# Kernel tuning notes

Hardware: AMD Instinct MI355X
Metric: run time of the kernel (lower is better)

The kernel has to match this reference:

```python
import jax, jax.numpy as jnp
import numpy as np

B, S, H = 128, 512, 768      # batch, seq, encoder hidden
NL = 42                      # len(LABEL_TO_ID)
LD = 300                     # label_dim
DK, DV = 64, 768             # K_dim, V_dim
HID = 768                    # opt['hidden_dim']
P = 512                      # max_seq_length == pos_indicator
INF = 1e12                   # constant.INFINITY_NUMBER
NEG = -1e9


def gelu(x):
    return 0.5 * x * (1.0 + jax.lax.erf(x * 0.7071067811865476))


def setup_inputs() -> dict:
    key = jax.random.key(0)
    ks = jax.random.split(key, 24)
    sc = 0.02
    return {
        "inputs": jax.random.normal(ks[0], (B, S, H), jnp.float32),
        "pos_ids": jax.random.randint(ks[1], (B, S), 0, 53),
        "dep_ids": jax.random.randint(ks[2], (B, S), 0, 42),
        "subj_pos": jax.random.randint(ks[3], (B, S), 0, P + 1),
        "obj_pos": jax.random.randint(ks[4], (B, S), 0, P + 1),
        "adj": jnp.zeros((1, 1, 1), jnp.float32),  # unused by forward
        # stacked per-label Q/K projections (41 = NL-1 labels, label 0 excluded)
        "WQ": jax.random.normal(ks[5], (NL - 1, DK, H), jnp.float32) * sc,
        "bQ": jax.random.normal(ks[6], (NL - 1, DK), jnp.float32) * sc,
        "WK": jax.random.normal(ks[7], (NL - 1, DK, LD), jnp.float32) * sc,
        "bK": jax.random.normal(ks[8], (NL - 1, DK), jnp.float32) * sc,
        "WV_w": jax.random.normal(ks[9], (DV, H), jnp.float32) * sc,
        "WV_b": jax.random.normal(ks[10], (DV,), jnp.float32) * sc,
        "Wout_w": jax.random.normal(ks[11], (H, DV), jnp.float32) * sc,
        "Wout_b": jax.random.normal(ks[12], (H,), jnp.float32) * sc,
        "ln_g": jnp.ones((H,), jnp.float32),
        "ln_b": jnp.zeros((H,), jnp.float32),
        "label_emb": jax.random.normal(ks[13], (NL, LD), jnp.float32) * sc,
        "feat_w": jax.random.normal(ks[14], (HID, 3 * H), jnp.float32) * sc,
        "feat_b": jax.random.normal(ks[15], (HID,), jnp.float32) * sc,
        "out_w": jax.random.normal(ks[16], (LD, HID), jnp.float32) * sc,
        "out_b": jax.random.normal(ks[17], (LD,), jnp.float32) * sc,
    }


def reference(inputs, pos_ids, dep_ids, subj_pos, obj_pos, adj,
              WQ, bQ, WK, bK, WV_w, WV_b, Wout_w, Wout_b, ln_g, ln_b,
              label_emb, feat_w, feat_b, out_w, out_b):
    dt = inputs.dtype
    # combined attention mask (bool OR, as torch bool+bool): entity markers + padding
    mask = (subj_pos == P) | (obj_pos == P) | (pos_ids == 0)   # [B,S]

    # --- LabelAttention: 41-loop collapses to one fused projection ---
    lab = label_emb[1:NL]                                      # [41,LD] labels 1..41
    kvec = jnp.einsum('ld,lkd->lk', lab, WK) + bK              # [41,DK] per-label keys
    # scores_sum[b,s] = sum_l (x W_Q_l^T + b_Q_l) . k_l  /sqrt(dk)  + 41*mask*NEG
    w_eff = jnp.einsum('lk,lkh->h', kvec, WQ)                  # [H]
    c = jnp.sum(kvec * bQ)                                     # scalar
    scores = (inputs @ w_eff + c) / 8.0                        # sqrt(DK)=8; [B,S]
    scores = scores + (NL - 1) * mask.astype(dt) * NEG
    attn = jax.nn.softmax(scores, axis=-1)                     # [B,S]

    wv = inputs @ WV_w.T + WV_b                                # [B,S,DV]
    ctx = jnp.einsum('bs,bsd->bd', attn, wv)                   # [B,DV]
    ctx = gelu(ctx @ Wout_w.T + Wout_b)                        # [B,H]
    mu = ctx.mean(-1, keepdims=True)
    var = ((ctx - mu) ** 2).mean(-1, keepdims=True)
    ctx = (ctx - mu) / jnp.sqrt(var + 1e-5) * ln_g + ln_b

    # --- entity max pooling (mask True where NOT part of entity) ---
    sm = (subj_pos != P)[:, :, None]
    om = (obj_pos != P)[:, :, None]
    subj_out = jnp.where(sm, -INF, inputs).max(axis=1)         # [B,H]
    obj_out = jnp.where(om, -INF, inputs).max(axis=1)          # [B,H]

    feats = jnp.concatenate([subj_out, obj_out, ctx], axis=-1)  # [B,3H]
    feats = gelu(feats @ feat_w.T + feat_b)                     # [B,HID]
    feats = gelu(feats @ out_w.T + out_b)                       # [B,LD]

    logits = feats @ label_emb.T                                # [B,42]
    return logits, ctx
```

## Files before the change

### kernel.cpp

```cpp
#include <hip/hip_runtime.h>
#include <math.h>

#define BB 128
#define SS 512
#define HH 768
#define PPOS 512
#define NEGC (-1.0e9f)
#define NINF (-1.0e12f)

#define OFF_KVEC   0
#define OFF_WEFF   2624
#define OFF_C      3392
#define OFF_CAT    0
#define OFF_POOLED 294912
#define OFF_PP     393216
#define OFF_PS     1179648
#define OFF_PO     1966080
#define OFF_PZ     2752512
#define OFF_CTXA   393216
#define OFF_CTXB   491520
#define OFF_F1     589824
#define OFF_F2     688128

__device__ __forceinline__ float gelu_f(float x) {
    return 0.5f * x * (1.0f + erff(x * 0.70710678118654752f));
}
__device__ __forceinline__ float dot4(float4 a, float4 b) {
    return a.x*b.x + a.y*b.y + a.z*b.z + a.w*b.w;
}

template<int K4, int ACT, int MT>
__global__ __launch_bounds__(256) void k_mm(const float* __restrict__ A,
        const float* __restrict__ W, const float* __restrict__ bias,
        float* __restrict__ C, int M, int N) {
    int lane = threadIdx.x & 63;
    int wave = (blockIdx.x * 256 + threadIdx.x) >> 6;
    int ntn = (N + 15) >> 4;
    int m0 = (wave / ntn) * MT;
    if (m0 >= M) return;
    int n0 = ((wave % ntn) << 4) + (lane >> 2);
    int ks = lane & 3;
    bool nvalid = (n0 < N);
    const float4* A4 = (const float4*)A;
    const float4* w_row = (const float4*)W + (size_t)(nvalid ? n0 : 0) * K4;
    const float4* ar = A4 + (size_t)m0 * K4;
    float acc[MT];
    #pragma unroll
    for (int r = 0; r < MT; ++r) acc[r] = 0.f;
    #pragma unroll 4
    for (int j = ks; j < K4; j += 4) {
        float4 wv = w_row[j];
        #pragma unroll
        for (int r = 0; r < MT; ++r) acc[r] += dot4(ar[(size_t)r * K4 + j], wv);
    }
    #pragma unroll
    for (int r = 0; r < MT; ++r) {
        acc[r] += __shfl_xor(acc[r], 1, 64);
        acc[r] += __shfl_xor(acc[r], 2, 64);
    }
    if (ks == 0 && nvalid) {
        float b = bias ? bias[n0] : 0.f;
        #pragma unroll
        for (int r = 0; r < MT; ++r) {
            float v = acc[r] + b;
            if (ACT == 1) v = gelu_f(v);
            C[(size_t)(m0 + r) * N + n0] = v;
        }
    }
}

template<int K4, int ACT>
__global__ __launch_bounds__(256) void k_mmX(const float* __restrict__ A,
        const float* __restrict__ W, const float* __restrict__ bias,
        float* __restrict__ C) {
    int lane = threadIdx.x & 63, wave = threadIdx.x >> 6;
    int x = blockIdx.x & 7;
    int k = blockIdx.x >> 3;
    int nb = x * 6 + (k % 6);
    int mb = k / 6;
    int m0 = mb * 8 + wave * 2;
    int n_sub = lane >> 2, ks = lane & 3;
    int n0 = (nb << 4) + n_sub;
    const float4* w_row = (const float4*)W + (size_t)n0 * K4;
    const float4* ar = (const float4*)A + (size_t)m0 * K4;
    float acc0 = 0.f, acc1 = 0.f;
    #pragma unroll 4
    for (int j = ks; j < K4; j += 4) {
        float4 wv = w_row[j];
        acc0 += dot4(ar[j], wv);
        acc1 += dot4(ar[K4 + j], wv);
    }
    acc0 += __shfl_xor(acc0, 1, 64); acc0 += __shfl_xor(acc0, 2, 64);
    acc1 += __shfl_xor(acc1, 1, 64); acc1 += __shfl_xor(acc1, 2, 64);
    if (ks == 0) {
        float b = bias ? bias[n0] : 0.f;
        float v0 = acc0 + b, v1 = acc1 + b;
        if (ACT == 1) { v0 = gelu_f(v0); v1 = gelu_f(v1); }
        C[(size_t)m0 * HH + n0] = v0;
        C[(size_t)(m0 + 1) * HH + n0] = v1;
    }
}

__global__ __launch_bounds__(256) void k_kvec2(const float* __restrict__ label_emb,
        const float* __restrict__ WK, const float* __restrict__ bK,
        float* __restrict__ ws) {
    if (blockIdx.x < 3) ws[OFF_WEFF + blockIdx.x * 256 + threadIdx.x] = 0.f;
    if (blockIdx.x == 3 && threadIdx.x == 0) ws[OFF_C] = 0.f;
    int lane = threadIdx.x & 63;
    int idx = (blockIdx.x * 256 + threadIdx.x) >> 6;
    int l = idx >> 6;
    const float4* lab4 = (const float4*)(label_emb + (size_t)(l + 1) * 300);
    const float4* wk4  = (const float4*)(WK + (size_t)idx * 300);
    float acc = dot4(lab4[lane], wk4[lane]);
    if (lane < 11) acc += dot4(lab4[64 + lane], wk4[64 + lane]);
    #pragma unroll
    for (int off = 32; off > 0; off >>= 1) acc += __shfl_xor(acc, off, 64);
    if (lane == 0) ws[OFF_KVEC + idx] = acc + bK[idx];
}

__global__ __launch_bounds__(256) void k_weff2(const float* __restrict__ WQ,
        const float* __restrict__ bQ, float* __restrict__ ws) {
    int lane = threadIdx.x & 63;
    int w = (blockIdx.x * 256 + threadIdx.x) >> 6;
    if (w < 492) {
        int jc = w / 12, hg = w % 12;
        int h = hg * 64 + lane;
        const float* wq = WQ + (size_t)(jc * 64) * HH + h;
        const float* kv = ws + OFF_KVEC + jc * 64;
        float acc = 0.f;
        #pragma unroll 8
        for (int j = 0; j < 64; ++j) acc += kv[j] * wq[(size_t)j * HH];
        atomicAdd(&ws[OFF_WEFF + h], acc);
    } else if (w == 492) {
        float acc = 0.f;
        for (int j = lane; j < 2624; j += 64) acc += ws[OFF_KVEC + j] * bQ[j];
        #pragma unroll
        for (int off = 32; off > 0; off >>= 1) acc += __shfl_xor(acc, off, 64);
        if (lane == 0) atomicAdd(&ws[OFF_C], acc);
    }
}

__global__ __launch_bounds__(256) void k_fused(const float* __restrict__ inputs,
        const int* __restrict__ pos_ids, const int* __restrict__ subj_pos,
        const int* __restrict__ obj_pos, float* __restrict__ ws) {
    __shared__ float l_pe[4][768];
    __shared__ float l_sm[4][768];
    __shared__ float l_om[4][768];
    __shared__ float l_z[4];
    __shared__ int l_mask[64];
    int chunk = blockIdx.x, b = blockIdx.y;
    int t = threadIdx.x, wave = t >> 6, lane = t & 63;
    int row0 = b * SS + chunk * 64;
    if (t < 64) {
        int g = row0 + t;
        int sp = subj_pos[g], op = obj_pos[g], pi = pos_ids[g];
        int m = ((sp == PPOS) | (op == PPOS) | (pi == 0)) ? 1 : 0;
        if (sp == PPOS) m |= 2;
        if (op == PPOS) m |= 4;
        l_mask[t] = m;
    }
    const float4* w4 = (const float4*)(ws + OFF_WEFF);
    float c = ws[OFF_C];
    float4 w0 = w4[lane], w1 = w4[64 + lane], w2 = w4[128 + lane];
    __syncthreads();
    const float4* in4 = (const float4*)inputs;
    float4 pe0 = make_float4(0.f, 0.f, 0.f, 0.f);
    float4 pe1 = pe0, pe2 = pe0;
    float4 sm0 = make_float4(NINF, NINF, NINF, NINF);
    float4 sm1 = sm0, sm2 = sm0, om0 = sm0, om1 = sm0, om2 = sm0;
    float z = 0.f;
    int rbase = wave * 16;
    #pragma unroll 4
    for (int r = 0; r < 16; ++r) {
        int s = rbase + r;
        const float4* x4 = in4 + (size_t)(row0 + s) * 192;
        float4 x0 = x4[lane], x1 = x4[64 + lane], x2 = x4[128 + lane];
        float acc = dot4(x0, w0) + dot4(x1, w1) + dot4(x2, w2);
        #pragma unroll
        for (int off = 32; off > 0; off >>= 1) acc += __shfl_xor(acc, off, 64);
        int mk = l_mask[s];
        float e = (mk & 1) ? 0.f : __expf((acc + c) * 0.125f);
        z += e;
        pe0.x += e * x0.x; pe0.y += e * x0.y; pe0.z += e * x0.z; pe0.w += e * x0.w;
        pe1.x += e * x1.x; pe1.y += e * x1.y; pe1.z += e * x1.z; pe1.w += e * x1.w;
        pe2.x += e * x2.x; pe2.y += e * x2.y; pe2.z += e * x2.z; pe2.w += e * x2.w;
        if (mk & 2) {
            sm0.x = fmaxf(sm0.x, x0.x); sm0.y = fmaxf(sm0.y, x0.y);
            sm0.z = fmaxf(sm0.z, x0.z); sm0.w = fmaxf(sm0.w, x0.w);
            sm1.x = fmaxf(sm1.x, x1.x); sm1.y = fmaxf(sm1.y, x1.y);
            sm1.z = fmaxf(sm1.z, x1.z); sm1.w = fmaxf(sm1.w, x1.w);
            sm2.x = fmaxf(sm2.x, x2.x); sm2.y = fmaxf(sm2.y, x2.y);
            sm2.z = fmaxf(sm2.z, x2.z); sm2.w = fmaxf(sm2.w, x2.w);
        }
        if (mk & 4) {
            om0.x = fmaxf(om0.x, x0.x); om0.y = fmaxf(om0.y, x0.y);
            om0.z = fmaxf(om0.z, x0.z); om0.w = fmaxf(om0.w, x0.w);
            om1.x = fmaxf(om1.x, x1.x); om1.y = fmaxf(om1.y, x1.y);
            om1.z = fmaxf(om1.z, x1.z); om1.w = fmaxf(om1.w, x1.w);
            om2.x = fmaxf(om2.x, x2.x); om2.y = fmaxf(om2.y, x2.y);
            om2.z = fmaxf(om2.z, x2.z); om2.w = fmaxf(om2.w, x2.w);
        }
    }
    ((float4*)l_pe[wave])[lane] = pe0;
    ((float4*)l_pe[wave])[64 + lane] = pe1;
    ((float4*)l_pe[wave])[128 + lane] = pe2;
    ((float4*)l_sm[wave])[lane] = sm0;
    ((float4*)l_sm[wave])[64 + lane] = sm1;
    ((float4*)l_sm[wave])[128 + lane] = sm2;
    ((float4*)l_om[wave])[lane] = om0;
    ((float4*)l_om[wave])[64 + lane] = om1;
    ((float4*)l_om[wave])[128 + lane] = om2;
    if (lane == 0) l_z[wave] = z;
    __syncthreads();
    if (t < 192) {
        float4 p = make_float4(0.f, 0.f, 0.f, 0.f);
        float4 s = make_float4(NINF, NINF, NINF, NINF);
        float4 o = s;
        #pragma unroll
        for (int w = 0; w < 4; ++w) {
            float4 vp = ((float4*)l_pe[w])[t];
            float4 vs = ((float4*)l_sm[w])[t];
            float4 vo = ((float4*)l_om[w])[t];
            p.x += vp.x; p.y += vp.y; p.z += vp.z; p.w += vp.w;
            s.x = fmaxf(s.x, vs.x); s.y = fmaxf(s.y, vs.y);
            s.z = fmaxf(s.z, vs.z); s.w = fmaxf(s.w, vs.w);
            o.x = fmaxf(o.x, vo.x); o.y = fmaxf(o.y, vo.y);
            o.z = fmaxf(o.z, vo.z); o.w = fmaxf(o.w, vo.w);
        }
        size_t oo = (size_t)(b * 8 + chunk) * 192 + t;
        ((float4*)(ws + OFF_PP))[oo] = p;
        ((float4*)(ws + OFF_PS))[oo] = s;
        ((float4*)(ws + OFF_PO))[oo] = o;
    }
    if (t == 0) ws[OFF_PZ + b * 8 + chunk] = l_z[0] + l_z[1] + l_z[2] + l_z[3];
}

__global__ void k_reduce(float* __restrict__ ws) {
    int i = blockIdx.x * 256 + threadIdx.x;
    int b = i / HH, h = i - b * HH;
    float p = 0.f, sm = NINF, om = NINF, zt = 0.f;
    #pragma unroll
    for (int j = 0; j < 8; ++j) {
        int o = (b * 8 + j) * HH + h;
        p += ws[OFF_PP + o];
        sm = fmaxf(sm, ws[OFF_PS + o]);
        om = fmaxf(om, ws[OFF_PO + o]);
        zt += ws[OFF_PZ + b * 8 + j];
    }
    ws[OFF_POOLED + i] = p / zt;
    ws[OFF_CAT + (size_t)b * 2304 + h] = sm;
    ws[OFF_CAT + (size_t)b * 2304 + 768 + h] = om;
}

__global__ void k_ln(const float* __restrict__ ln_g, const float* __restrict__ ln_b,
                     float* __restrict__ ws, float* __restrict__ out) {
    __shared__ float red[256];
    __shared__ float red2[256];
    int b = blockIdx.x, t = threadIdx.x;
    const float* x = ws + OFF_CTXB + (size_t)b * HH;
    float a0 = x[t], a1 = x[t + 256], a2 = x[t + 512];
    red[t]  = a0 + a1 + a2;
    red2[t] = a0 * a0 + a1 * a1 + a2 * a2;
    __syncthreads();
    for (int s2 = 128; s2 > 0; s2 >>= 1) {
        if (t < s2) { red[t] += red[t + s2]; red2[t] += red2[t + s2]; }
        __syncthreads();
    }
    float mu  = red[0] * (1.0f / 768.0f);
    float var = red2[0] * (1.0f / 768.0f) - mu * mu;
    float inv = rsqrtf(var + 1e-5f);
    float* o = out + 5376 + (size_t)b * HH;
    float* cc = ws + OFF_CAT + (size_t)b * 2304 + 1536;
    float r0 = (a0 - mu) * inv * ln_g[t]       + ln_b[t];
    float r1 = (a1 - mu) * inv * ln_g[t + 256] + ln_b[t + 256];
    float r2 = (a2 - mu) * inv * ln_g[t + 512] + ln_b[t + 512];
    o[t] = r0; o[t + 256] = r1; o[t + 512] = r2;
    cc[t] = r0; cc[t + 256] = r1; cc[t + 512] = r2;
}

extern "C" void kernel_launch(void* const* d_in, const int* in_sizes, int n_in,
                              void* d_out, int out_size, void* d_ws, size_t ws_size,
                              hipStream_t stream) {
    const float* inputs    = (const float*)d_in[0];
    const int*   pos_ids   = (const int*)d_in[1];
    const int*   subj_pos  = (const int*)d_in[3];
    const int*   obj_pos   = (const int*)d_in[4];
    const float* WQ        = (const float*)d_in[6];
    const float* bQ        = (const float*)d_in[7];
    const float* WK        = (const float*)d_in[8];
    const float* bK        = (const float*)d_in[9];
    const float* WV_w      = (const float*)d_in[10];
    const float* WV_b      = (const float*)d_in[11];
    const float* Wout_w    = (const float*)d_in[12];
    const float* Wout_b    = (const float*)d_in[13];
    const float* ln_g      = (const float*)d_in[14];
    const float* ln_b      = (const float*)d_in[15];
    const float* label_emb = (const float*)d_in[16];
    const float* feat_w    = (const float*)d_in[17];
    const float* feat_b    = (const float*)d_in[18];
    const float* out_w     = (const float*)d_in[19];
    const float* out_b     = (const float*)d_in[20];
    float* out = (float*)d_out;
    float* ws  = (float*)d_ws;

    k_kvec2  <<<656, 256, 0, stream>>>(label_emb, WK, bK, ws);
    k_weff2  <<<124, 256, 0, stream>>>(WQ, bQ, ws);
    k_fused  <<<dim3(8, BB), 256, 0, stream>>>(inputs, pos_ids, subj_pos, obj_pos, ws);
    k_reduce <<<384, 256, 0, stream>>>(ws);
    k_mmX<192,0><<<768, 256, 0, stream>>>(ws + OFF_POOLED, WV_w, WV_b, ws + OFF_CTXA);
    k_mmX<192,1><<<768, 256, 0, stream>>>(ws + OFF_CTXA, Wout_w, Wout_b, ws + OFF_CTXB);
    k_ln     <<<BB, 256, 0, stream>>>(ln_g, ln_b, ws, out);
    k_mmX<576,1><<<768, 256, 0, stream>>>(ws + OFF_CAT, feat_w, feat_b, ws + OFF_F1);
    k_mm<192,1,2><<<304, 256, 0, stream>>>(ws + OFF_F1, out_w, out_b, ws + OFF_F2, BB, 300);
    k_mm<75,0,2><<<48, 256, 0, stream>>>(ws + OFF_F2, label_emb, nullptr, out, BB, 42);
}
```

Measured before the change: 450.2 us.

## Replace partial-buffer reduce kernel with atomic accumulation in fused pass

Removes the k_reduce kernel and its partial buffers. The fused kernel now atomically adds pooled sums and softmax denominators and does an atomicMax on order-preserving uint keys for the entity max pools. Entity max updates are skipped when a chunk has no masked rows. Workspace initialisation moves into the kvec kernel, key decoding into the LN kernel, and division by Z into the first matmul epilogue. This saves one launch and the partial-buffer traffic, at the cost of atomic contention and nondeterministic summation order.

```diff
diff --git a/kernel.cpp b/kernel.cpp
--- a/kernel.cpp
+++ b/kernel.cpp
@@ -5,28 +5,34 @@
 #define SS 512
 #define HH 768
 #define PPOS 512
-#define NEGC (-1.0e9f)
 #define NINF (-1.0e12f)
 
 #define OFF_KVEC   0
 #define OFF_WEFF   2624
 #define OFF_C      3392
-#define OFF_CAT    0
+#define OFF_Z      3456
 #define OFF_POOLED 294912
-#define OFF_PP     393216
-#define OFF_PS     1179648
-#define OFF_PO     1966080
-#define OFF_PZ     2752512
-#define OFF_CTXA   393216
-#define OFF_CTXB   491520
-#define OFF_F1     589824
-#define OFF_F2     688128
+#define OFF_CAT    393216
+#define OFF_CTXA   688128
+#define OFF_CTXB   786432
+#define OFF_F1     884736
+#define OFF_F2     983040
+
+#define N_INIT 295040
+#define INIT_THREADS 167936
 
 __device__ __forceinline__ float gelu_f(float x) {
     return 0.5f * x * (1.0f + erff(x * 0.70710678118654752f));
 }
 __device__ __forceinline__ float dot4(float4 a, float4 b) {
     return a.x*b.x + a.y*b.y + a.z*b.z + a.w*b.w;
+}
+__device__ __forceinline__ unsigned fkey(float f) {
+    unsigned u = __float_as_uint(f);
+    return (u & 0x80000000u) ? ~u : (u | 0x80000000u);
+}
+__device__ __forceinline__ float fkey_dec(unsigned k) {
+    return __uint_as_float((k & 0x80000000u) ? (k & 0x7fffffffu) : ~k);
 }
 
 template<int K4, int ACT, int MT>
@@ -72,7 +78,7 @@
 template<int K4, int ACT>
 __global__ __launch_bounds__(256) void k_mmX(const float* __restrict__ A,
         const float* __restrict__ W, const float* __restrict__ bias,
-        float* __restrict__ C) {
+        float* __restrict__ C, const float* __restrict__ Zv) {
     int lane = threadIdx.x & 63, wave = threadIdx.x >> 6;
     int x = blockIdx.x & 7;
     int k = blockIdx.x >> 3;
@@ -94,7 +100,14 @@
     acc1 += __shfl_xor(acc1, 1, 64); acc1 += __shfl_xor(acc1, 2, 64);
     if (ks == 0) {
         float b = bias ? bias[n0] : 0.f;
-        float v0 = acc0 + b, v1 = acc1 + b;
+        float v0, v1;
+        if (Zv) {
+            v0 = acc0 * (1.f / Zv[m0]) + b;
+            v1 = acc1 * (1.f / Zv[m0 + 1]) + b;
+        } else {
+            v0 = acc0 + b;
+            v1 = acc1 + b;
+        }
         if (ACT == 1) { v0 = gelu_f(v0); v1 = gelu_f(v1); }
         C[(size_t)m0 * HH + n0] = v0;
         C[(size_t)(m0 + 1) * HH + n0] = v1;
@@ -106,6 +119,17 @@
         float* __restrict__ ws) {
     if (blockIdx.x < 3) ws[OFF_WEFF + blockIdx.x * 256 + threadIdx.x] = 0.f;
     if (blockIdx.x == 3 && threadIdx.x == 0) ws[OFF_C] = 0.f;
+    unsigned keyn = fkey(NINF);
+    int tid = blockIdx.x * 256 + threadIdx.x;
+    for (int idx = tid; idx < N_INIT; idx += INIT_THREADS) {
+        if (idx < 98304) ws[OFF_POOLED + idx] = 0.f;
+        else if (idx < 98432) ws[OFF_Z + (idx - 98304)] = 0.f;
+        else {
+            int cidx = idx - 98432;
+            int b = cidx / 1536, off = cidx - b * 1536;
+            ((unsigned*)ws)[OFF_CAT + b * 2304 + off] = keyn;
+        }
+    }
     int lane = threadIdx.x & 63;
     int idx = (blockIdx.x * 256 + threadIdx.x) >> 6;
     int l = idx >> 6;
@@ -148,6 +172,7 @@
     __shared__ float l_om[4][768];
     __shared__ float l_z[4];
     __shared__ int l_mask[64];
+    __shared__ int sflag, oflag;
     int chunk = blockIdx.x, b = blockIdx.y;
     int t = threadIdx.x, wave = t >> 6, lane = t & 63;
     int row0 = b * SS + chunk * 64;
@@ -158,6 +183,9 @@
         if (sp == PPOS) m |= 2;
         if (op == PPOS) m |= 4;
         l_mask[t] = m;
+        unsigned long long bs = __ballot((m & 2) != 0);
+        unsigned long long bo = __ballot((m & 4) != 0);
+        if (t == 0) { sflag = bs ? 1 : 0; oflag = bo ? 1 : 0; }
     }
     const float4* w4 = (const float4*)(ws + OFF_WEFF);
     float c = ws[OFF_C];
@@ -227,29 +255,22 @@
             o.x = fmaxf(o.x, vo.x); o.y = fmaxf(o.y, vo.y);
             o.z = fmaxf(o.z, vo.z); o.w = fmaxf(o.w, vo.w);
         }
-        size_t oo = (size_t)(b * 8 + chunk) * 192 + t;
-        ((float4*)(ws + OFF_PP))[oo] = p;
-        ((float4*)(ws + OFF_PS))[oo] = s;
-        ((float4*)(ws + OFF_PO))[oo] = o;
-    }
-    if (t == 0) ws[OFF_PZ + b * 8 + chunk] = l_z[0] + l_z[1] + l_z[2] + l_z[3];
-}
-
-__global__ void k_reduce(float* __restrict__ ws) {
-    int i = blockIdx.x * 256 + threadIdx.x;
-    int b = i / HH, h = i - b * HH;
-    float p = 0.f, sm = NINF, om = NINF, zt = 0.f;
-    #pragma unroll
-    for (int j = 0; j < 8; ++j) {
-        int o = (b * 8 + j) * HH + h;
-        p += ws[OFF_PP + o];
-        sm = fmaxf(sm, ws[OFF_PS + o]);
-        om = fmaxf(om, ws[OFF_PO + o]);
-        zt += ws[OFF_PZ + b * 8 + j];
-    }
-    ws[OFF_POOLED + i] = p / zt;
-    ws[OFF_CAT + (size_t)b * 2304 + h] = sm;
-    ws[OFF_CAT + (size_t)b * 2304 + 768 + h] = om;
+        int hb = t * 4;
+        float* pooled = ws + OFF_POOLED + (size_t)b * HH + hb;
+        atomicAdd(&pooled[0], p.x); atomicAdd(&pooled[1], p.y);
+        atomicAdd(&pooled[2], p.z); atomicAdd(&pooled[3], p.w);
+        if (sflag) {
+            unsigned* sk = (unsigned*)ws + OFF_CAT + (size_t)b * 2304 + hb;
+            atomicMax(&sk[0], fkey(s.x)); atomicMax(&sk[1], fkey(s.y));
+            atomicMax(&sk[2], fkey(s.z)); atomicMax(&sk[3], fkey(s.w));
+        }
+        if (oflag) {
+            unsigned* ok = (unsigned*)ws + OFF_CAT + (size_t)b * 2304 + 768 + hb;
+            atomicMax(&ok[0], fkey(o.x)); atomicMax(&ok[1], fkey(o.y));
+            atomicMax(&ok[2], fkey(o.z)); atomicMax(&ok[3], fkey(o.w));
+        }
+    }
+    if (t == 0) atomicAdd(&ws[OFF_Z + b], l_z[0] + l_z[1] + l_z[2] + l_z[3]);
 }
 
 __global__ void k_ln(const float* __restrict__ ln_g, const float* __restrict__ ln_b,
@@ -257,6 +278,10 @@
     __shared__ float red[256];
     __shared__ float red2[256];
     int b = blockIdx.x, t = threadIdx.x;
+    unsigned* ck = (unsigned*)ws + OFF_CAT + (size_t)b * 2304;
+    #pragma unroll
+    for (int i = t; i < 1536; i += 256)
+        ((float*)ck)[i] = fkey_dec(ck[i]);
     const float* x = ws + OFF_CTXB + (size_t)b * HH;
     float a0 = x[t], a1 = x[t + 256], a2 = x[t + 512];
     red[t]  = a0 + a1 + a2;
@@ -306,11 +331,10 @@
     k_kvec2  <<<656, 256, 0, stream>>>(label_emb, WK, bK, ws);
     k_weff2  <<<124, 256, 0, stream>>>(WQ, bQ, ws);
     k_fused  <<<dim3(8, BB), 256, 0, stream>>>(inputs, pos_ids, subj_pos, obj_pos, ws);
-    k_reduce <<<384, 256, 0, stream>>>(ws);
-    k_mmX<192,0><<<768, 256, 0, stream>>>(ws + OFF_POOLED, WV_w, WV_b, ws + OFF_CTXA);
-    k_mmX<192,1><<<768, 256, 0, stream>>>(ws + OFF_CTXA, Wout_w, Wout_b, ws + OFF_CTXB);
+    k_mmX<192,0><<<768, 256, 0, stream>>>(ws + OFF_POOLED, WV_w, WV_b, ws + OFF_CTXA, ws + OFF_Z);
+    k_mmX<192,1><<<768, 256, 0, stream>>>(ws + OFF_CTXA, Wout_w, Wout_b, ws + OFF_CTXB, nullptr);
     k_ln     <<<BB, 256, 0, stream>>>(ln_g, ln_b, ws, out);
-    k_mmX<576,1><<<768, 256, 0, stream>>>(ws + OFF_CAT, feat_w, feat_b, ws + OFF_F1);
+    k_mmX<576,1><<<768, 256, 0, stream>>>(ws + OFF_CAT, feat_w, feat_b, ws + OFF_F1, nullptr);
     k_mm<192,1,2><<<304, 256, 0, stream>>>(ws + OFF_F1, out_w, out_b, ws + OFF_F2, BB, 300);
     k_mm<75,0,2><<<48, 256, 0, stream>>>(ws + OFF_F2, label_emb, nullptr, out, BB, 42);
 }
```

Result: no change. 449.9 us (-0.1%).
